# Optimization experiments

Hardware: AMD Instinct MI355X
Metric: run time of the kernel (lower is better)

Reference implementation:

```python
import jax, jax.numpy as jnp
import numpy as np

B, T, D = 128, 2048, 256


def setup_inputs() -> dict:
    key = jax.random.key(0)
    ks = jax.random.split(key, 6)
    s = 1.0 / np.sqrt(D)  # kaiming-uniform-ish scale for bias-free Linear
    return {
        "x": jax.random.normal(ks[0], (B, T, D), jnp.float32),
        "W_in": jax.random.normal(ks[1], (D, D), jnp.float32) * s,
        "W_select": jax.random.normal(ks[2], (D, D), jnp.float32) * s,
        "W_gate": jax.random.normal(ks[3], (D, D), jnp.float32) * s,
        "W_out": jax.random.normal(ks[4], (D, D), jnp.float32) * s,
        "W_delta": jax.random.normal(ks[5], (D, D), jnp.float32) * s,
        "log_a": jnp.zeros((D,), jnp.float32),  # module inits log_a = zeros
    }


def _diag_recurrence(decay, update):
    # state_t = decay_t * state_{t-1} + update_t, state_{-1} = 0 (zero-init fast path)
    # First-order linear recurrence as an associative scan:
    # (a1,b1) o (a2,b2) = (a1*a2, a2*b1 + b2)
    def combine(c1, c2):
        a1, b1 = c1
        a2, b2 = c2
        return a1 * a2, a2 * b1 + b2

    _, states = jax.lax.associative_scan(combine, (decay, update), axis=1)
    return states  # (B, T, D)


def reference(x, W_in, W_select, W_gate, W_out, W_delta, log_a):
    # selective diag-SSM (a_mode='diag'):
    #   delta  = softplus(delta_proj(x))                  timestep / selectivity
    #   decay  = exp(-delta * exp(log_a))                 in (0, 1]
    #   update = delta * sigmoid(select_proj(x)) * in_proj(x)
    #   states = scan(state = decay*state + update)
    #   y      = states * silu(gate_proj(x)); out = out_proj(y)
    delta = jax.nn.softplus(jnp.einsum("btd,ed->bte", x, W_delta))
    decay = jnp.exp(-delta * jnp.exp(log_a))
    u = jnp.einsum("btd,ed->bte", x, W_in)
    sel = jax.nn.sigmoid(jnp.einsum("btd,ed->bte", x, W_select))
    update = delta * sel * u
    states = _diag_recurrence(decay, update)
    gate = jax.nn.silu(jnp.einsum("btd,ed->bte", x, W_gate))
    return jnp.einsum("btd,ed->bte", states * gate, W_out)
```

## Files before the change

### kernel.cpp

```cpp
#include <hip/hip_runtime.h>
#include <hip/hip_bf16.h>
#include <hip/hip_fp16.h>
#include <math.h>


typedef __attribute__((ext_vector_type(8))) short s16x8;
typedef __attribute__((ext_vector_type(4))) float f32x4;
typedef __attribute__((ext_vector_type(4))) unsigned short u16x4;

#define D_DIM 256
#define T_DIM 2048
#define B_DIM 128
#define NCHUNK 16
#define CLEN 128
#define ROWB 528

__device__ __forceinline__ unsigned short f2bf(float f) {
    union { float f; unsigned int u; } v; v.f = f;
    unsigned int r = v.u + 0x7fffu + ((v.u >> 16) & 1u);
    return (unsigned short)(r >> 16);
}
__device__ __forceinline__ float bf2f(unsigned short s) {
    union { unsigned int u; float f; } v; v.u = ((unsigned int)s) << 16;
    return v.f;
}
__device__ __forceinline__ s16x8 cvt8(const float* xp) {
    float4 p0 = *(const float4*)xp;
    float4 p1 = *(const float4*)(xp + 4);
    s16x8 a;
    a[0] = (short)f2bf(p0.x); a[1] = (short)f2bf(p0.y);
    a[2] = (short)f2bf(p0.z); a[3] = (short)f2bf(p0.w);
    a[4] = (short)f2bf(p1.x); a[5] = (short)f2bf(p1.y);
    a[6] = (short)f2bf(p1.z); a[7] = (short)f2bf(p1.w);
    return a;
}

__global__ __launch_bounds__(256) void prep_kernel(
    const float* __restrict__ W_in, const float* __restrict__ W_select,
    const float* __restrict__ W_gate, const float* __restrict__ W_out,
    const float* __restrict__ W_delta, const float* __restrict__ log_a,
    unsigned short* __restrict__ Wb, float* __restrict__ ea)
{
    int i = blockIdx.x * 256 + threadIdx.x;
    if (i < 5 * 65536) {
        int s = i >> 16, j = i & 65535;
        const float* src = (s == 0) ? W_delta : (s == 1) ? W_select
                         : (s == 2) ? W_in    : (s == 3) ? W_gate : W_out;
        Wb[i] = f2bf(src[j]);
    } else if (i < 5 * 65536 + 256) {
        int j = i - 5 * 65536;
        ea[j] = expf(log_a[j]);
    }
}

__global__ __launch_bounds__(256, 3) void gemm_du_kernel(
    const float* __restrict__ x, const unsigned short* __restrict__ Wb,
    const float* __restrict__ ea, __half2* __restrict__ du)
{
    __shared__ unsigned short xls[64 * (ROWB / 2)];
    int bid = blockIdx.x;
    int wg  = (bid & 7) * (8192 / 8) + (bid >> 3);
    int mtile = wg >> 1;
    int ntile = wg & 1;
    int tid  = threadIdx.x;
    int lane = tid & 63, wid = tid >> 6;
    int mbase = mtile * 64;

#pragma unroll
    for (int i = 0; i < 8; ++i) {
        int e = i * 256 + tid;
        int r = e >> 5, g = e & 31;
        s16x8 a = cvt8(x + (size_t)(mbase + r) * D_DIM + g * 8);
        *(s16x8*)((char*)xls + r * ROWB + g * 16) = a;
    }
    __syncthreads();

    int l16 = lane & 15;
    int lk  = lane >> 4;
    int n0  = ntile * 128 + wid * 32;

    f32x4 acc[3][4][2] = {};

    for (int ks = 0; ks < 8; ++ks) {
        int kb = ks * 32 + lk * 8;
        s16x8 xf[4];
#pragma unroll
        for (int mf = 0; mf < 4; ++mf)
            xf[mf] = *(const s16x8*)((const char*)xls + (mf * 16 + l16) * ROWB
                                     + (ks * 4 + lk) * 16);
#pragma unroll
        for (int w = 0; w < 3; ++w) {
#pragma unroll
            for (int nf = 0; nf < 2; ++nf) {
                s16x8 wfr = *(const s16x8*)(
                    Wb + ((size_t)w << 16) + (size_t)(n0 + nf * 16 + l16) * D_DIM + kb);
#pragma unroll
                for (int mf = 0; mf < 4; ++mf)
                    acc[w][mf][nf] = __builtin_amdgcn_mfma_f32_16x16x32_bf16(
                        wfr, xf[mf], acc[w][mf][nf], 0, 0, 0);
            }
        }
    }

    int r0 = lk * 4;
#pragma unroll
    for (int mf = 0; mf < 4; ++mf) {
        int m = mbase + mf * 16 + l16;
#pragma unroll
        for (int nf = 0; nf < 2; ++nf) {
            int n = n0 + nf * 16 + r0;
            float4 eav = *(const float4*)(ea + n);
            __half2 dv[4];
#pragma unroll
            for (int j = 0; j < 4; ++j) {
                float ad = acc[0][mf][nf][j];
                float as = acc[1][mf][nf][j];
                float ai = acc[2][mf][nf][j];
                float e = __expf(ad);
                float delta = (ad > 15.f) ? ad : __logf(1.f + e);
                float ean = (j == 0) ? eav.x : (j == 1) ? eav.y : (j == 2) ? eav.z : eav.w;
                float dec = __expf(-delta * ean);
                float sel = 1.f / (1.f + __expf(-as));
                float upd = delta * sel * ai;
                dv[j] = __floats2half2_rn(dec, upd);
            }
            *(f32x4*)(du + (size_t)m * D_DIM + n) = *(f32x4*)dv;
        }
    }
}

__global__ __launch_bounds__(256, 4) void gemm_gate_kernel(
    const float* __restrict__ x, const unsigned short* __restrict__ Wg,
    unsigned short* __restrict__ gate)
{
    __shared__ unsigned short xls[64 * (ROWB / 2)];
    int bid = blockIdx.x;
    int wg  = (bid & 7) * (4096 / 8) + (bid >> 3);
    int mbase = wg * 64;
    int tid  = threadIdx.x;
    int lane = tid & 63, wid = tid >> 6;

#pragma unroll
    for (int i = 0; i < 8; ++i) {
        int e = i * 256 + tid;
        int r = e >> 5, g = e & 31;
        s16x8 a = cvt8(x + (size_t)(mbase + r) * D_DIM + g * 8);
        *(s16x8*)((char*)xls + r * ROWB + g * 16) = a;
    }
    __syncthreads();

    int l16 = lane & 15;
    int lk  = lane >> 4;
    int n0  = wid * 64;

    f32x4 acc[4][4] = {};

    for (int ks = 0; ks < 8; ++ks) {
        int kb = ks * 32 + lk * 8;
        s16x8 xf[4];
#pragma unroll
        for (int mf = 0; mf < 4; ++mf)
            xf[mf] = *(const s16x8*)((const char*)xls + (mf * 16 + l16) * ROWB
                                     + (ks * 4 + lk) * 16);
#pragma unroll
        for (int nf = 0; nf < 4; ++nf) {
            s16x8 wfr = *(const s16x8*)(
                Wg + (size_t)(n0 + nf * 16 + l16) * D_DIM + kb);
#pragma unroll
            for (int mf = 0; mf < 4; ++mf)
                acc[mf][nf] = __builtin_amdgcn_mfma_f32_16x16x32_bf16(
                    wfr, xf[mf], acc[mf][nf], 0, 0, 0);
        }
    }

    int r0 = lk * 4;
#pragma unroll
    for (int mf = 0; mf < 4; ++mf) {
        int m = mbase + mf * 16 + l16;
#pragma unroll
        for (int nf = 0; nf < 4; ++nf) {
            int n = n0 + nf * 16 + r0;
            u16x4 gv;
#pragma unroll
            for (int j = 0; j < 4; ++j) {
                float ag = acc[mf][nf][j];
                gv[j] = f2bf(ag / (1.f + __expf(-ag)));
            }
            *(u16x4*)(gate + (size_t)m * D_DIM + n) = gv;
        }
    }
}

__global__ __launch_bounds__(256) void scan1_kernel(
    const __half2* __restrict__ du,
    float* __restrict__ cA, float* __restrict__ cS)
{
    int b = blockIdx.x >> 4;
    int c = blockIdx.x & 15;
    int d = threadIdx.x;
    size_t base = ((size_t)b * T_DIM + (size_t)c * CLEN) * D_DIM + d;
    float A = 1.f, S = 0.f;
#pragma unroll 4
    for (int t = 0; t < CLEN; ++t) {
        __half2 v = du[base + (size_t)t * D_DIM];
        float dc = __low2float(v);
        float up = __high2float(v);
        A *= dc;
        S = fmaf(dc, S, up);
    }
    int idx = (b * NCHUNK + c) * D_DIM + d;
    cA[idx] = A;
    cS[idx] = S;
}

__global__ __launch_bounds__(256) void scan2_kernel(
    const float* __restrict__ cA, const float* __restrict__ cS,
    float* __restrict__ carry)
{
    int b = blockIdx.x;
    int d = threadIdx.x;
    float s = 0.f;
    for (int c = 0; c < NCHUNK; ++c) {
        int idx = (b * NCHUNK + c) * D_DIM + d;
        carry[idx] = s;
        s = fmaf(cA[idx], s, cS[idx]);
    }
}

__global__ __launch_bounds__(256) void scan_out_kernel(
    const __half2* __restrict__ du, const unsigned short* __restrict__ gate,
    const float* __restrict__ carry, const unsigned short* __restrict__ Wo,
    float* __restrict__ out)
{
    __shared__ unsigned short yls[128 * 256];
    int b = blockIdx.x >> 4;
    int c = blockIdx.x & 15;
    int tid = threadIdx.x;

    {
        int d = tid;
        size_t base = ((size_t)b * T_DIM + (size_t)c * CLEN) * D_DIM + d;
        float s = carry[(b * NCHUNK + c) * D_DIM + d];
        int dlo = d & 7, dch = d >> 3;
#pragma unroll 4
        for (int t = 0; t < CLEN; ++t) {
            __half2 v = du[base + (size_t)t * D_DIM];
            float dc = __low2float(v);
            float up = __high2float(v);
            s = fmaf(dc, s, up);
            float g = bf2f(gate[base + (size_t)t * D_DIM]);
            int off = t * 256 + ((dch ^ (t & 7)) << 3) + dlo;
            yls[off] = f2bf(s * g);
        }
    }
    __syncthreads();

    int lane = tid & 63, wid = tid >> 6;
    int l16 = lane & 15;
    int lkc = lane >> 4;
    int m0 = (wid >> 1) * 64;
    size_t rbase = (size_t)b * T_DIM + (size_t)c * CLEN;
    int r0 = lkc * 4;

    for (int nblk = 0; nblk < 2; ++nblk) {
        int n0 = (wid & 1) * 64 + nblk * 128;
        f32x4 acc[4][4] = {};
        for (int ks = 0; ks < 8; ++ks) {
            int kb = ks * 32 + lkc * 8;
            s16x8 yf[4];
#pragma unroll
            for (int mf = 0; mf < 4; ++mf) {
                int row = m0 + mf * 16 + l16;
                int chunk = (ks * 4 + lkc) ^ (row & 7);
                yf[mf] = *(const s16x8*)&yls[row * 256 + chunk * 8];
            }
#pragma unroll
            for (int nf = 0; nf < 4; ++nf) {
                s16x8 wfr = *(const s16x8*)(Wo + (size_t)(n0 + nf * 16 + l16) * D_DIM + kb);
#pragma unroll
                for (int mf = 0; mf < 4; ++mf)
                    acc[mf][nf] = __builtin_amdgcn_mfma_f32_16x16x32_bf16(
                        wfr, yf[mf], acc[mf][nf], 0, 0, 0);
            }
        }
#pragma unroll
        for (int mf = 0; mf < 4; ++mf) {
            size_t rowg = rbase + m0 + mf * 16 + l16;
#pragma unroll
            for (int nf = 0; nf < 4; ++nf) {
                int n = n0 + nf * 16 + r0;
                *(f32x4*)(out + rowg * D_DIM + n) = acc[mf][nf];
            }
        }
    }
}

extern "C" void kernel_launch(void* const* d_in, const int* in_sizes, int n_in,
                              void* d_out, int out_size, void* d_ws, size_t ws_size,
                              hipStream_t stream)
{
    const float* x        = (const float*)d_in[0];
    const float* W_in     = (const float*)d_in[1];
    const float* W_select = (const float*)d_in[2];
    const float* W_gate   = (const float*)d_in[3];
    const float* W_out    = (const float*)d_in[4];
    const float* W_delta  = (const float*)d_in[5];
    const float* log_a    = (const float*)d_in[6];
    float* out = (float*)d_out;

    char* ws = (char*)d_ws;
    const size_t MB = 1ull << 20;
    unsigned short* Wb    = (unsigned short*)(ws);
    float*          ea    = (float*)(ws + 655360);
    __half2*        du    = (__half2*)(ws + 1 * MB);
    unsigned short* gate  = (unsigned short*)(ws + 257 * MB);
    float*          cA    = (float*)(ws + 385 * MB);
    float*          cS    = (float*)(ws + 387 * MB);
    float*          carry = (float*)(ws + 389 * MB);

    prep_kernel<<<1281, 256, 0, stream>>>(W_in, W_select, W_gate, W_out,
                                          W_delta, log_a, Wb, ea);
    gemm_du_kernel<<<8192, 256, 0, stream>>>(x, Wb, ea, du);
    gemm_gate_kernel<<<4096, 256, 0, stream>>>(x, Wb + 3 * 65536, gate);
    scan1_kernel<<<B_DIM * NCHUNK, 256, 0, stream>>>(du, cA, cS);
    scan2_kernel<<<B_DIM, 256, 0, stream>>>(cA, cS, carry);
    scan_out_kernel<<<B_DIM * NCHUNK, 256, 0, stream>>>(du, gate, carry,
                                                        Wb + 4 * 65536, out);
}
```

Before: 718.4 us.

## Make projection GEMMs persistent with register prefetch of next x tile

The two projection GEMM kernels become persistent: a fixed grid of 1024 blocks loops over several tiles instead of launching one block per tile. Each iteration issues the global loads for the next x tile into registers while the current tile is computed, hiding load latency behind the MFMA work. Outputs are written with nontemporal stores to avoid polluting cache. Occupancy hints drop to 2 blocks per CU, and the extra prefetch registers add pressure; the bid swizzle for L2 locality is removed.

Result: slower. 854.3 us (+18.9%).

```diff
diff --git a/kernel.cpp b/kernel.cpp
--- a/kernel.cpp
+++ b/kernel.cpp
@@ -15,6 +15,11 @@
 #define CLEN 128
 #define ROWB 528
 
+#define GRID_DU 1024
+#define TILES_DU 8
+#define GRID_G  1024
+#define TILES_G 4
+
 __device__ __forceinline__ unsigned short f2bf(float f) {
     union { float f; unsigned int u; } v; v.f = f;
     unsigned int r = v.u + 0x7fffu + ((v.u >> 16) & 1u);
@@ -24,9 +29,7 @@
     union { unsigned int u; float f; } v; v.u = ((unsigned int)s) << 16;
     return v.f;
 }
-__device__ __forceinline__ s16x8 cvt8(const float* xp) {
-    float4 p0 = *(const float4*)xp;
-    float4 p1 = *(const float4*)(xp + 4);
+__device__ __forceinline__ s16x8 cvt2(float4 p0, float4 p1) {
     s16x8 a;
     a[0] = (short)f2bf(p0.x); a[1] = (short)f2bf(p0.y);
     a[2] = (short)f2bf(p0.z); a[3] = (short)f2bf(p0.w);
@@ -53,140 +56,191 @@
     }
 }
 
-__global__ __launch_bounds__(256, 3) void gemm_du_kernel(
+__global__ __launch_bounds__(256, 2) void gemm_du_kernel(
     const float* __restrict__ x, const unsigned short* __restrict__ Wb,
     const float* __restrict__ ea, __half2* __restrict__ du)
 {
     __shared__ unsigned short xls[64 * (ROWB / 2)];
-    int bid = blockIdx.x;
-    int wg  = (bid & 7) * (8192 / 8) + (bid >> 3);
-    int mtile = wg >> 1;
-    int ntile = wg & 1;
     int tid  = threadIdx.x;
     int lane = tid & 63, wid = tid >> 6;
-    int mbase = mtile * 64;
+    int l16 = lane & 15, lk = lane >> 4;
+
+    float4 pf[8][2];
 
 #pragma unroll
     for (int i = 0; i < 8; ++i) {
-        int e = i * 256 + tid;
-        int r = e >> 5, g = e & 31;
-        s16x8 a = cvt8(x + (size_t)(mbase + r) * D_DIM + g * 8);
-        *(s16x8*)((char*)xls + r * ROWB + g * 16) = a;
-    }
-    __syncthreads();
-
-    int l16 = lane & 15;
-    int lk  = lane >> 4;
-    int n0  = ntile * 128 + wid * 32;
-
-    f32x4 acc[3][4][2] = {};
-
-    for (int ks = 0; ks < 8; ++ks) {
-        int kb = ks * 32 + lk * 8;
-        s16x8 xf[4];
-#pragma unroll
-        for (int mf = 0; mf < 4; ++mf)
-            xf[mf] = *(const s16x8*)((const char*)xls + (mf * 16 + l16) * ROWB
-                                     + (ks * 4 + lk) * 16);
-#pragma unroll
-        for (int w = 0; w < 3; ++w) {
+        int e = i * 256 + tid, r = e >> 5, g = e & 31;
+        const float* xp = x + (size_t)(((int)blockIdx.x >> 1) * 64 + r) * D_DIM + g * 8;
+        pf[i][0] = *(const float4*)xp;
+        pf[i][1] = *(const float4*)(xp + 4);
+    }
+
+#pragma unroll 1
+    for (int it = 0; it < TILES_DU; ++it) {
+        int tile  = it * GRID_DU + blockIdx.x;
+        int mbase = (tile >> 1) * 64;
+        int ntile = tile & 1;
+
+        s16x8 st[8];
+#pragma unroll
+        for (int i = 0; i < 8; ++i) st[i] = cvt2(pf[i][0], pf[i][1]);
+
+        __syncthreads();
+#pragma unroll
+        for (int i = 0; i < 8; ++i) {
+            int e = i * 256 + tid, r = e >> 5, g = e & 31;
+            *(s16x8*)((char*)xls + r * ROWB + g * 16) = st[i];
+        }
+        if (it + 1 < TILES_DU) {
+            int mb2 = (((it + 1) * GRID_DU + blockIdx.x) >> 1) * 64;
+#pragma unroll
+            for (int i = 0; i < 8; ++i) {
+                int e = i * 256 + tid, r = e >> 5, g = e & 31;
+                const float* xp = x + (size_t)(mb2 + r) * D_DIM + g * 8;
+                pf[i][0] = *(const float4*)xp;
+                pf[i][1] = *(const float4*)(xp + 4);
+            }
+        }
+        __syncthreads();
+
+        int n0 = ntile * 128 + wid * 32;
+        f32x4 acc[3][4][2] = {};
+
+#pragma unroll
+        for (int ks = 0; ks < 8; ++ks) {
+            int kb = ks * 32 + lk * 8;
+            s16x8 xf[4];
+#pragma unroll
+            for (int mf = 0; mf < 4; ++mf)
+                xf[mf] = *(const s16x8*)((const char*)xls + (mf * 16 + l16) * ROWB
+                                         + (ks * 4 + lk) * 16);
+#pragma unroll
+            for (int w = 0; w < 3; ++w) {
+#pragma unroll
+                for (int nf = 0; nf < 2; ++nf) {
+                    s16x8 wfr = *(const s16x8*)(
+                        Wb + ((size_t)w << 16) + (size_t)(n0 + nf * 16 + l16) * D_DIM + kb);
+#pragma unroll
+                    for (int mf = 0; mf < 4; ++mf)
+                        acc[w][mf][nf] = __builtin_amdgcn_mfma_f32_16x16x32_bf16(
+                            wfr, xf[mf], acc[w][mf][nf], 0, 0, 0);
+                }
+            }
+        }
+
+        int r0 = lk * 4;
+#pragma unroll
+        for (int mf = 0; mf < 4; ++mf) {
+            int m = mbase + mf * 16 + l16;
 #pragma unroll
             for (int nf = 0; nf < 2; ++nf) {
-                s16x8 wfr = *(const s16x8*)(
-                    Wb + ((size_t)w << 16) + (size_t)(n0 + nf * 16 + l16) * D_DIM + kb);
-#pragma unroll
-                for (int mf = 0; mf < 4; ++mf)
-                    acc[w][mf][nf] = __builtin_amdgcn_mfma_f32_16x16x32_bf16(
-                        wfr, xf[mf], acc[w][mf][nf], 0, 0, 0);
-            }
-        }
-    }
-
-    int r0 = lk * 4;
-#pragma unroll
-    for (int mf = 0; mf < 4; ++mf) {
-        int m = mbase + mf * 16 + l16;
-#pragma unroll
-        for (int nf = 0; nf < 2; ++nf) {
-            int n = n0 + nf * 16 + r0;
-            float4 eav = *(const float4*)(ea + n);
-            __half2 dv[4];
-#pragma unroll
-            for (int j = 0; j < 4; ++j) {
-                float ad = acc[0][mf][nf][j];
-                float as = acc[1][mf][nf][j];
-                float ai = acc[2][mf][nf][j];
-                float e = __expf(ad);
-                float delta = (ad > 15.f) ? ad : __logf(1.f + e);
-                float ean = (j == 0) ? eav.x : (j == 1) ? eav.y : (j == 2) ? eav.z : eav.w;
-                float dec = __expf(-delta * ean);
-                float sel = 1.f / (1.f + __expf(-as));
-                float upd = delta * sel * ai;
-                dv[j] = __floats2half2_rn(dec, upd);
-            }
-            *(f32x4*)(du + (size_t)m * D_DIM + n) = *(f32x4*)dv;
-        }
-    }
-}
-
-__global__ __launch_bounds__(256, 4) void gemm_gate_kernel(
+                int n = n0 + nf * 16 + r0;
+                float4 eav = *(const float4*)(ea + n);
+                __half2 dv[4];
+#pragma unroll
+                for (int j = 0; j < 4; ++j) {
+                    float ad = acc[0][mf][nf][j];
+                    float as = acc[1][mf][nf][j];
+                    float ai = acc[2][mf][nf][j];
+                    float e = __expf(ad);
+                    float delta = (ad > 15.f) ? ad : __logf(1.f + e);
+                    float ean = (j == 0) ? eav.x : (j == 1) ? eav.y
+                              : (j == 2) ? eav.z : eav.w;
+                    float dec = __expf(-delta * ean);
+                    float sel = 1.f / (1.f + __expf(-as));
+                    float upd = delta * sel * ai;
+                    dv[j] = __floats2half2_rn(dec, upd);
+                }
+                __builtin_nontemporal_store(*(f32x4*)dv,
+                                            (f32x4*)(du + (size_t)m * D_DIM + n));
+            }
+        }
+    }
+}
+
+__global__ __launch_bounds__(256, 2) void gemm_gate_kernel(
     const float* __restrict__ x, const unsigned short* __restrict__ Wg,
     unsigned short* __restrict__ gate)
 {
     __shared__ unsigned short xls[64 * (ROWB / 2)];
-    int bid = blockIdx.x;
-    int wg  = (bid & 7) * (4096 / 8) + (bid >> 3);
-    int mbase = wg * 64;
     int tid  = threadIdx.x;
     int lane = tid & 63, wid = tid >> 6;
+    int l16 = lane & 15, lk = lane >> 4;
+
+    float4 pf[8][2];
 
 #pragma unroll
     for (int i = 0; i < 8; ++i) {
-        int e = i * 256 + tid;
-        int r = e >> 5, g = e & 31;
-        s16x8 a = cvt8(x + (size_t)(mbase + r) * D_DIM + g * 8);
-        *(s16x8*)((char*)xls + r * ROWB + g * 16) = a;
-    }
-    __syncthreads();
-
-    int l16 = lane & 15;
-    int lk  = lane >> 4;
-    int n0  = wid * 64;
-
-    f32x4 acc[4][4] = {};
-
-    for (int ks = 0; ks < 8; ++ks) {
-        int kb = ks * 32 + lk * 8;
-        s16x8 xf[4];
-#pragma unroll
-        for (int mf = 0; mf < 4; ++mf)
-            xf[mf] = *(const s16x8*)((const char*)xls + (mf * 16 + l16) * ROWB
-                                     + (ks * 4 + lk) * 16);
-#pragma unroll
-        for (int nf = 0; nf < 4; ++nf) {
-            s16x8 wfr = *(const s16x8*)(
-                Wg + (size_t)(n0 + nf * 16 + l16) * D_DIM + kb);
+        int e = i * 256 + tid, r = e >> 5, g = e & 31;
+        const float* xp = x + (size_t)((int)blockIdx.x * 64 + r) * D_DIM + g * 8;
+        pf[i][0] = *(const float4*)xp;
+        pf[i][1] = *(const float4*)(xp + 4);
+    }
+
+#pragma unroll 1
+    for (int it = 0; it < TILES_G; ++it) {
+        int mbase = (it * GRID_G + blockIdx.x) * 64;
+
+        s16x8 st[8];
+#pragma unroll
+        for (int i = 0; i < 8; ++i) st[i] = cvt2(pf[i][0], pf[i][1]);
+
+        __syncthreads();
+#pragma unroll
+        for (int i = 0; i < 8; ++i) {
+            int e = i * 256 + tid, r = e >> 5, g = e & 31;
+            *(s16x8*)((char*)xls + r * ROWB + g * 16) = st[i];
+        }
+        if (it + 1 < TILES_G) {
+            int mb2 = ((it + 1) * GRID_G + blockIdx.x) * 64;
+#pragma unroll
+            for (int i = 0; i < 8; ++i) {
+                int e = i * 256 + tid, r = e >> 5, g = e & 31;
+                const float* xp = x + (size_t)(mb2 + r) * D_DIM + g * 8;
+                pf[i][0] = *(const float4*)xp;
+                pf[i][1] = *(const float4*)(xp + 4);
+            }
+        }
+        __syncthreads();
+
+        int n0 = wid * 64;
+        f32x4 acc[4][4] = {};
+
+#pragma unroll
+        for (int ks = 0; ks < 8; ++ks) {
+            int kb = ks * 32 + lk * 8;
+            s16x8 xf[4];
 #pragma unroll
             for (int mf = 0; mf < 4; ++mf)
-                acc[mf][nf] = __builtin_amdgcn_mfma_f32_16x16x32_bf16(
-                    wfr, xf[mf], acc[mf][nf], 0, 0, 0);
-        }
-    }
-
-    int r0 = lk * 4;
-#pragma unroll
-    for (int mf = 0; mf < 4; ++mf) {
-        int m = mbase + mf * 16 + l16;
-#pragma unroll
-        for (int nf = 0; nf < 4; ++nf) {
-            int n = n0 + nf * 16 + r0;
-            u16x4 gv;
-#pragma unroll
-            for (int j = 0; j < 4; ++j) {
-                float ag = acc[mf][nf][j];
-                gv[j] = f2bf(ag / (1.f + __expf(-ag)));
-            }
-            *(u16x4*)(gate + (size_t)m * D_DIM + n) = gv;
+                xf[mf] = *(const s16x8*)((const char*)xls + (mf * 16 + l16) * ROWB
+                                         + (ks * 4 + lk) * 16);
+#pragma unroll
+            for (int nf = 0; nf < 4; ++nf) {
+                s16x8 wfr = *(const s16x8*)(
+                    Wg + (size_t)(n0 + nf * 16 + l16) * D_DIM + kb);
+#pragma unroll
+                for (int mf = 0; mf < 4; ++mf)
+                    acc[mf][nf] = __builtin_amdgcn_mfma_f32_16x16x32_bf16(
+                        wfr, xf[mf], acc[mf][nf], 0, 0, 0);
+            }
+        }
+
+        int r0 = lk * 4;
+#pragma unroll
+        for (int mf = 0; mf < 4; ++mf) {
+            int m = mbase + mf * 16 + l16;
+#pragma unroll
+            for (int nf = 0; nf < 4; ++nf) {
+                int n = n0 + nf * 16 + r0;
+                u16x4 gv;
+#pragma unroll
+                for (int j = 0; j < 4; ++j) {
+                    float ag = acc[mf][nf][j];
+                    gv[j] = f2bf(ag / (1.f + __expf(-ag)));
+                }
+                __builtin_nontemporal_store(gv,
+                    (u16x4*)(gate + (size_t)m * D_DIM + n));
+            }
         }
     }
 }
@@ -320,8 +374,8 @@
 
     prep_kernel<<<1281, 256, 0, stream>>>(W_in, W_select, W_gate, W_out,
                                           W_delta, log_a, Wb, ea);
-    gemm_du_kernel<<<8192, 256, 0, stream>>>(x, Wb, ea, du);
-    gemm_gate_kernel<<<4096, 256, 0, stream>>>(x, Wb + 3 * 65536, gate);
+    gemm_du_kernel<<<GRID_DU, 256, 0, stream>>>(x, Wb, ea, du);
+    gemm_gate_kernel<<<GRID_G, 256, 0, stream>>>(x, Wb + 3 * 65536, gate);
     scan1_kernel<<<B_DIM * NCHUNK, 256, 0, stream>>>(du, cA, cS);
     scan2_kernel<<<B_DIM, 256, 0, stream>>>(cA, cS, carry);
     scan_out_kernel<<<B_DIM * NCHUNK, 256, 0, stream>>>(du, gate, carry,
```
